# Kernel tuning notes

Measured on AMD Instinct MI355X. Metric: run time of the kernel, lower is better.

Reference implementation:

```python
import jax, jax.numpy as jnp
import numpy as np

CH = 512
HEADS = 8
REDUCTION = 2
INNER = max(CH // REDUCTION, HEADS)  # 256
POS_RES = 16
LN_EPS = 1e-5


def setup_inputs() -> dict:
    key = jax.random.key(0)
    ks = jax.random.split(key, 7)
    B, H, W = 1, 64, 64
    x = jax.random.normal(ks[0], (B, CH, H, W), dtype=jnp.float32)
    w_qkv = jax.random.normal(ks[1], (INNER * 3, CH), dtype=jnp.float32) * 0.02
    w_proj = jax.random.normal(ks[2], (CH, INNER), dtype=jnp.float32) * 0.02
    b_proj = jnp.zeros((CH,), dtype=jnp.float32)
    pos_bias = jax.random.normal(ks[3], (1, HEADS, POS_RES, POS_RES), dtype=jnp.float32) * 0.02
    gamma = jnp.ones((CH,), dtype=jnp.float32)
    beta = jnp.zeros((CH,), dtype=jnp.float32)
    return {"x": x, "w_qkv": w_qkv, "w_proj": w_proj, "b_proj": b_proj,
            "pos_bias": pos_bias, "gamma": gamma, "beta": beta}


def reference(x, w_qkv, w_proj, b_proj, pos_bias, gamma, beta):
    B, C, H, W = x.shape
    d_head = INNER // HEADS
    scale = jnp.float32(d_head ** -0.5)

    # 1x1 conv == channel matmul
    qkv = jnp.einsum('oc,bchw->bohw', w_qkv, x)  # [B, 3*inner, H, W]
    q, k, v = jnp.split(qkv, 3, axis=1)

    def heads_view(t):
        return t.reshape(B, HEADS, d_head, H * W)  # [B, h, d, HW]

    q, k, v = heads_view(q), heads_view(k), heads_view(v)

    attn = jnp.einsum('bhdi,bhdj->bhij', q * scale, k)  # [B, h, HW, HW]

    # bilinear interp of pos bias 16x16 -> HxW (half-pixel, matches align_corners=False)
    pos = jax.image.resize(pos_bias, (1, HEADS, H, W), method='bilinear')
    pos = pos.reshape(1, HEADS, H * W)
    attn = attn + pos[..., :, None] + pos[..., None, :]

    attn = jax.nn.softmax(attn, axis=-1)
    y = jnp.einsum('bhij,bhdj->bhdi', attn, v)  # [B, h, d, HW]
    y = y.reshape(B, INNER, H, W)

    y = jnp.einsum('co,bohw->bchw', w_proj, y) + b_proj[None, :, None, None]

    # LayerNorm over channel dim of (x + y)
    z = (x + y).transpose(0, 2, 3, 1)  # [B, H, W, C]
    mu = jnp.mean(z, axis=-1, keepdims=True)
    var = jnp.var(z, axis=-1, keepdims=True)
    z = (z - mu) / jnp.sqrt(var + LN_EPS) * gamma + beta
    return z.transpose(0, 3, 1, 2)
```

## Files before the change

### kernel.cpp

```cpp
#include <hip/hip_runtime.h>
#include <hip/hip_bf16.h>
#include <math.h>

#define HW 4096
#define LN_EPS 1e-5f

typedef _Float16 half4v __attribute__((ext_vector_type(4)));
typedef _Float16 half8v __attribute__((ext_vector_type(8)));
typedef float float4v __attribute__((ext_vector_type(4)));
typedef __fp16 fp16v2 __attribute__((ext_vector_type(2)));
typedef __fp16 fp16v4 __attribute__((ext_vector_type(4)));

#if __has_builtin(__builtin_amdgcn_exp2f)
#define EXP2F(x) __builtin_amdgcn_exp2f(x)
#else
#define EXP2F(x) exp2f(x)
#endif

__device__ __forceinline__ half4v lo4(half8v v) { return __builtin_shufflevector(v, v, 0, 1, 2, 3); }
__device__ __forceinline__ half4v hi4(half8v v) { return __builtin_shufflevector(v, v, 4, 5, 6, 7); }

__device__ __forceinline__ void gload_lds16(const _Float16* g, _Float16* l) {
#if __has_builtin(__builtin_amdgcn_global_load_lds)
    __builtin_amdgcn_global_load_lds(
        (const __attribute__((address_space(1))) void*)(const void*)g,
        (__attribute__((address_space(3))) void*)(void*)l, 16, 0, 0);
#else
    int lane = threadIdx.x & 63;
    *(half8v*)(l + lane * 8) = *(const half8v*)g;
#endif
}

__global__ __launch_bounds__(256) void k_pre(const float* __restrict__ x,
                                             const float* __restrict__ wq,
                                             const float* __restrict__ wp,
                                             const float* __restrict__ pb,
                                             _Float16* __restrict__ xt,
                                             _Float16* __restrict__ wqh,
                                             _Float16* __restrict__ wph,
                                             float* __restrict__ pos) {
    int bx = blockIdx.x, t = threadIdx.x;
    if (bx < 512) {
        __shared__ _Float16 tile[64][65];
        int c0 = (bx >> 6) * 64, p0 = (bx & 63) * 64;
        int w = t >> 6, lane = t & 63;
        #pragma unroll
        for (int r = 0; r < 16; r++)
            tile[w * 16 + r][lane] = (_Float16)x[(c0 + w * 16 + r) * HW + p0 + lane];
        __syncthreads();
        int cg = (t & 15) * 4, pr = t >> 4;
        #pragma unroll
        for (int r = 0; r < 4; r++) {
            int p = pr + r * 16;
            half4v v;
            #pragma unroll
            for (int k = 0; k < 4; k++) v[k] = tile[cg + k][p];
            *(half4v*)&xt[(p0 + p) * 512 + c0 + cg] = v;
        }
        return;
    }
    int i = (bx - 512) * 256 + t;
    const float qs = 0.17677669529663687f * 1.4426950408889634f;
    if (i < 49152) {
        float s = (i < 16384) ? qs : 1.0f;
        float4v a = *(const float4v*)(wq + i * 8);
        float4v b = *(const float4v*)(wq + i * 8 + 4);
        half8v h;
        #pragma unroll
        for (int k = 0; k < 4; k++) { h[k] = (_Float16)(a[k] * s); h[4 + k] = (_Float16)(b[k] * s); }
        *(half8v*)(wqh + i * 8) = h;
    } else if (i < 65536) {
        int j = i - 49152;
        float4v a = *(const float4v*)(wp + j * 8);
        float4v b = *(const float4v*)(wp + j * 8 + 4);
        half8v h;
        #pragma unroll
        for (int k = 0; k < 4; k++) { h[k] = (_Float16)a[k]; h[4 + k] = (_Float16)b[k]; }
        *(half8v*)(wph + j * 8) = h;
    } else {
        int j = i - 65536;
        int h = j >> 12, p = j & 4095, y = p >> 6, xx = p & 63;
        float sy = y * 0.25f - 0.375f, sx = xx * 0.25f - 0.375f;
        float fy = floorf(sy), fx = floorf(sx);
        float wy = sy - fy, wx = sx - fx;
        int y0 = (int)fy, x0 = (int)fx;
        int y1 = y0 + 1 < 15 ? y0 + 1 : 15;
        int x1 = x0 + 1 < 15 ? x0 + 1 : 15;
        y0 = y0 > 0 ? y0 : 0;
        x0 = x0 > 0 ? x0 : 0;
        const float* src = pb + h * 256;
        float v = (1.f - wy) * ((1.f - wx) * src[y0 * 16 + x0] + wx * src[y0 * 16 + x1]) +
                  wy * ((1.f - wx) * src[y1 * 16 + x0] + wx * src[y1 * 16 + x1]);
        pos[j] = v * 1.4426950408889634f;
    }
}

__global__ __launch_bounds__(256) void k_qkv(const _Float16* __restrict__ wqh,
                                             const _Float16* __restrict__ xt,
                                             _Float16* __restrict__ qa,
                                             _Float16* __restrict__ ka,
                                             _Float16* __restrict__ va) {
    int n0 = (blockIdx.x >> 5) * 64;
    int p0 = (blockIdx.x & 31) * 128;
    int t = threadIdx.x, w = t >> 6, lane = t & 63, quad = lane >> 4, l16 = lane & 15;

    const _Float16* aptr0 = xt + (p0 + w * 16 + l16) * 512 + quad * 8;
    const _Float16* aptr1 = aptr0 + 64 * 512;
    const _Float16* bptr = wqh + (n0 + l16) * 512 + quad * 8;

    float4v acc[2][4] = {};
    #pragma unroll 4
    for (int kc = 0; kc < 16; kc++) {
        half8v a0 = *(const half8v*)(aptr0 + kc * 32);
        half8v a1 = *(const half8v*)(aptr1 + kc * 32);
        #pragma unroll
        for (int nt = 0; nt < 4; nt++) {
            half8v b = *(const half8v*)(bptr + nt * 16 * 512 + kc * 32);
            acc[0][nt] = __builtin_amdgcn_mfma_f32_16x16x32_f16(a0, b, acc[0][nt], 0, 0, 0);
            acc[1][nt] = __builtin_amdgcn_mfma_f32_16x16x32_f16(a1, b, acc[1][nt], 0, 0, 0);
        }
    }
    #pragma unroll
    for (int ps = 0; ps < 2; ps++) {
        #pragma unroll
        for (int nt = 0; nt < 4; nt++) {
            int o = n0 + nt * 16 + l16;
            #pragma unroll
            for (int r = 0; r < 4; r++) {
                int p = p0 + ps * 64 + w * 16 + quad * 4 + r;
                _Float16 v = (_Float16)acc[ps][nt][r];
                if (o < 256) {
                    qa[(o >> 5) * 131072 + p * 32 + (o & 31)] = v;
                } else if (o < 512) {
                    int oc = o - 256, hh = oc >> 5, d = oc & 31;
                    ka[hh * 131072 + (p >> 4) * 512 + ((d >> 3) * 16 + (p & 15)) * 8 + (d & 7)] = v;
                } else {
                    int oc = o - 512, hh = oc >> 5, d = oc & 31;
                    va[hh * 131072 + (p >> 4) * 512 + (((p >> 2) & 3) * 16 + (d & 15)) * 8 +
                       (d >> 4) * 4 + (p & 3)] = v;
                }
            }
        }
    }
}

__global__ __launch_bounds__(256, 4) void k_attn(const _Float16* __restrict__ qa,
                                                 const _Float16* __restrict__ ka,
                                                 const _Float16* __restrict__ va,
                                                 const float* __restrict__ pos,
                                                 float* __restrict__ op,
                                                 float* __restrict__ lp) {
    __shared__ __attribute__((aligned(16))) _Float16 kbuf[2][2048];
    __shared__ __attribute__((aligned(16))) _Float16 vbuf[2][2048];
    __shared__ __attribute__((aligned(16))) float posl[1024];
    int h = blockIdx.x & 7;
    int jq = (blockIdx.x >> 3) & 3;
    int qb = blockIdx.x >> 5;
    int t = threadIdx.x, w = t >> 6, lane = t & 63, quad = lane >> 4, l16 = lane & 15;
    int q0 = qb * 128 + w * 32;

    float* opp = op + jq * 1048576;
    float* lpp = lp + jq * 32768;

    *(float4v*)(posl + t * 4) = *(const float4v*)(pos + h * HW + jq * 1024 + t * 4);

    half8v qf0 = *(const half8v*)(qa + h * 131072 + (q0 + l16) * 32 + quad * 8);
    half8v qf1 = *(const half8v*)(qa + h * 131072 + (q0 + 16 + l16) * 32 + quad * 8);

    const _Float16* kg = ka + h * 131072 + jq * 32768;
    const _Float16* vg = va + h * 131072 + jq * 32768;

    gload_lds16(kg + (w * 64 + lane) * 8, &kbuf[0][w * 512]);
    gload_lds16(vg + (w * 64 + lane) * 8, &vbuf[0][w * 512]);

    float4v o00 = {}, o01 = {}, o10 = {}, o11 = {};
    float lsum0 = 0.f, lsum1 = 0.f;
    const fp16v2 one2 = {(__fp16)1.0f, (__fp16)1.0f};

    for (int tile = 0; tile < 16; tile++) {
        int buf = tile & 1;
        __syncthreads();
        if (tile + 1 < 16) {
            gload_lds16(kg + (tile + 1) * 2048 + (w * 64 + lane) * 8, &kbuf[buf ^ 1][w * 512]);
            gload_lds16(vg + (tile + 1) * 2048 + (w * 64 + lane) * 8, &vbuf[buf ^ 1][w * 512]);
        }
        #pragma unroll
        for (int w16 = 0; w16 < 4; w16++) {
            half8v kf = *(const half8v*)(kbuf[buf] + w16 * 512 + lane * 8);
            half8v vf = *(const half8v*)(vbuf[buf] + w16 * 512 + lane * 8);
            float4v pbv = *(const float4v*)(posl + tile * 64 + w16 * 16 + quad * 4);

            float4v s0 = __builtin_amdgcn_mfma_f32_16x16x32_f16(kf, qf0, pbv, 0, 0, 0);
            float4v s1 = __builtin_amdgcn_mfma_f32_16x16x32_f16(kf, qf1, pbv, 0, 0, 0);

            float e0 = EXP2F(s0[0]);
            float e1 = EXP2F(s0[1]);
            float e2 = EXP2F(s0[2]);
            float e3 = EXP2F(s0[3]);
            float f0 = EXP2F(s1[0]);
            float f1 = EXP2F(s1[1]);
            float f2 = EXP2F(s1[2]);
            float f3 = EXP2F(s1[3]);

            fp16v2 a01 = __builtin_amdgcn_cvt_pkrtz(e0, e1);
            fp16v2 a23 = __builtin_amdgcn_cvt_pkrtz(e2, e3);
            fp16v2 b01 = __builtin_amdgcn_cvt_pkrtz(f0, f1);
            fp16v2 b23 = __builtin_amdgcn_cvt_pkrtz(f2, f3);
            half4v pa0 = __builtin_bit_cast(half4v, __builtin_shufflevector(a01, a23, 0, 1, 2, 3));
            half4v pa1 = __builtin_bit_cast(half4v, __builtin_shufflevector(b01, b23, 0, 1, 2, 3));

#if __has_builtin(__builtin_amdgcn_fdot2)
            lsum0 = __builtin_amdgcn_fdot2(a01, one2, lsum0, false);
            lsum0 = __builtin_amdgcn_fdot2(a23, one2, lsum0, false);
            lsum1 = __builtin_amdgcn_fdot2(b01, one2, lsum1, false);
            lsum1 = __builtin_amdgcn_fdot2(b23, one2, lsum1, false);
#else
            lsum0 += (e0 + e1) + (e2 + e3);
            lsum1 += (f0 + f1) + (f2 + f3);
#endif
            o00 = __builtin_amdgcn_mfma_f32_16x16x16f16(pa0, lo4(vf), o00, 0, 0, 0);
            o01 = __builtin_amdgcn_mfma_f32_16x16x16f16(pa0, hi4(vf), o01, 0, 0, 0);
            o10 = __builtin_amdgcn_mfma_f32_16x16x16f16(pa1, lo4(vf), o10, 0, 0, 0);
            o11 = __builtin_amdgcn_mfma_f32_16x16x16f16(pa1, hi4(vf), o11, 0, 0, 0);
        }
    }
    lsum0 += __shfl_xor(lsum0, 16, 64);
    lsum0 += __shfl_xor(lsum0, 32, 64);
    lsum1 += __shfl_xor(lsum1, 16, 64);
    lsum1 += __shfl_xor(lsum1, 32, 64);
    #pragma unroll
    for (int r = 0; r < 4; r++) {
        int qr = quad * 4 + r;
        int qi0 = q0 + qr, qi1 = q0 + 16 + qr;
        opp[qi0 * 256 + h * 32 + l16] = o00[r];
        opp[qi0 * 256 + h * 32 + 16 + l16] = o01[r];
        opp[qi1 * 256 + h * 32 + l16] = o10[r];
        opp[qi1 * 256 + h * 32 + 16 + l16] = o11[r];
    }
    if (quad == 0) {
        lpp[(q0 + l16) * 8 + h] = lsum0;
        lpp[(q0 + 16 + l16) * 8 + h] = lsum1;
    }
}

__global__ __launch_bounds__(1024) void k_proj_ln(const _Float16* __restrict__ wph,
                                                  const float* __restrict__ op,
                                                  const float* __restrict__ lp,
                                                  const float* __restrict__ x,
                                                  const float* __restrict__ b_proj,
                                                  const float* __restrict__ gamma,
                                                  const float* __restrict__ beta,
                                                  float* __restrict__ out) {
    __shared__ __attribute__((aligned(16))) _Float16 ys[16 * 264];
    __shared__ float red[2][16][17];
    int p0 = blockIdx.x * 16;
    int t = threadIdx.x, w = t >> 6, lane = t & 63, quad = lane >> 4, l16 = lane & 15;
    {
        int p = t >> 6, cg = (t & 63) * 4;
        int pi = p0 + p;
        float4v a0 = *(const float4v*)(op + pi * 256 + cg);
        float4v a1 = *(const float4v*)(op + 1048576 + pi * 256 + cg);
        float4v a2 = *(const float4v*)(op + 2097152 + pi * 256 + cg);
        float4v a3 = *(const float4v*)(op + 3145728 + pi * 256 + cg);
        int hh = cg >> 5;
        float l = lp[pi * 8 + hh] + lp[32768 + pi * 8 + hh] +
                  lp[65536 + pi * 8 + hh] + lp[98304 + pi * 8 + hh];
        float inv = 1.f / l;
        half4v y;
        #pragma unroll
        for (int k = 0; k < 4; k++) y[k] = (_Float16)(((a0[k] + a1[k]) + (a2[k] + a3[k])) * inv);
        *(half4v*)(ys + p * 264 + cg) = y;
    }
    __syncthreads();
    float4v acc[2] = {};
    #pragma unroll
    for (int kc = 0; kc < 8; kc++) {
        half8v b = *(const half8v*)(ys + l16 * 264 + kc * 32 + quad * 8);
        #pragma unroll
        for (int mt = 0; mt < 2; mt++) {
            half8v a = *(const half8v*)(wph + (w * 32 + mt * 16 + l16) * 256 + kc * 32 + quad * 8);
            acc[mt] = __builtin_amdgcn_mfma_f32_16x16x32_f16(a, b, acc[mt], 0, 0, 0);
        }
    }
    int p = p0 + l16;
    float sum = 0.f, sumsq = 0.f;
    #pragma unroll
    for (int mt = 0; mt < 2; mt++)
        #pragma unroll
        for (int r = 0; r < 4; r++) {
            int c = w * 32 + mt * 16 + quad * 4 + r;
            float v = acc[mt][r] + b_proj[c] + x[c * HW + p];
            acc[mt][r] = v;
            sum += v;
            sumsq += v * v;
        }
    sum += __shfl_xor(sum, 16, 64);
    sum += __shfl_xor(sum, 32, 64);
    sumsq += __shfl_xor(sumsq, 16, 64);
    sumsq += __shfl_xor(sumsq, 32, 64);
    if (quad == 0) { red[0][w][l16] = sum; red[1][w][l16] = sumsq; }
    __syncthreads();
    float s0 = 0.f, s1 = 0.f;
    #pragma unroll
    for (int ww = 0; ww < 16; ww++) { s0 += red[0][ww][l16]; s1 += red[1][ww][l16]; }
    float mean = s0 * (1.f / 512.f);
    float var = s1 * (1.f / 512.f) - mean * mean;
    float rstd = rsqrtf(var + LN_EPS);
    #pragma unroll
    for (int mt = 0; mt < 2; mt++)
        #pragma unroll
        for (int r = 0; r < 4; r++) {
            int c = w * 32 + mt * 16 + quad * 4 + r;
            out[c * HW + p] = (acc[mt][r] - mean) * rstd * gamma[c] + beta[c];
        }
}

extern "C" void kernel_launch(void* const* d_in, const int* in_sizes, int n_in,
                              void* d_out, int out_size, void* d_ws, size_t ws_size,
                              hipStream_t stream) {
    const float* x      = (const float*)d_in[0];
    const float* w_qkv  = (const float*)d_in[1];
    const float* w_proj = (const float*)d_in[2];
    const float* b_proj = (const float*)d_in[3];
    const float* pos_b  = (const float*)d_in[4];
    const float* gamma  = (const float*)d_in[5];
    const float* beta   = (const float*)d_in[6];
    char* ws = (char*)d_ws;
    _Float16* xt  = (_Float16*)(ws);
    _Float16* qa  = (_Float16*)(ws + 4194304);
    _Float16* ka  = (_Float16*)(ws + 6291456);
    _Float16* va  = (_Float16*)(ws + 8388608);
    float*    op  = (float*)   (ws + 10485760);
    float*    lp  = (float*)   (ws + 27262976);
    float*    pos = (float*)   (ws + 27787264);
    _Float16* wqh = (_Float16*)(ws + 27918336);
    _Float16* wph = (_Float16*)(ws + 28704768);

    k_pre<<<896, 256, 0, stream>>>(x, w_qkv, w_proj, pos_b, xt, wqh, wph, pos);
    k_qkv<<<384, 256, 0, stream>>>(wqh, xt, qa, ka, va);
    k_attn<<<1024, 256, 0, stream>>>(qa, ka, va, pos, op, lp);
    k_proj_ln<<<256, 1024, 0, stream>>>(wph, op, lp, x, b_proj, gamma, beta, (float*)d_out);
}
```

Baseline: 140.3 us.

## Use 16x16x32 MFMA for PV by re-laying K/V in 32-key pairs, store partials in fp16

```diff
diff --git a/kernel.cpp b/kernel.cpp
--- a/kernel.cpp
+++ b/kernel.cpp
@@ -16,9 +16,6 @@
 #else
 #define EXP2F(x) exp2f(x)
 #endif
-
-__device__ __forceinline__ half4v lo4(half8v v) { return __builtin_shufflevector(v, v, 0, 1, 2, 3); }
-__device__ __forceinline__ half4v hi4(half8v v) { return __builtin_shufflevector(v, v, 4, 5, 6, 7); }
 
 __device__ __forceinline__ void gload_lds16(const _Float16* g, _Float16* l) {
 #if __has_builtin(__builtin_amdgcn_global_load_lds)
@@ -133,11 +130,16 @@
                     qa[(o >> 5) * 131072 + p * 32 + (o & 31)] = v;
                 } else if (o < 512) {
                     int oc = o - 256, hh = oc >> 5, d = oc & 31;
-                    ka[hh * 131072 + (p >> 4) * 512 + ((d >> 3) * 16 + (p & 15)) * 8 + (d & 7)] = v;
+                    int p5 = p & 31, pair = p >> 5;
+                    int window = (p5 >> 2) & 1;
+                    int localrow = (p5 >> 3) * 4 + (p5 & 3);
+                    ka[hh * 131072 + (pair * 2 + window) * 512 +
+                       ((d >> 3) * 16 + localrow) * 8 + (d & 7)] = v;
                 } else {
                     int oc = o - 512, hh = oc >> 5, d = oc & 31;
-                    va[hh * 131072 + (p >> 4) * 512 + (((p >> 2) & 3) * 16 + (d & 15)) * 8 +
-                       (d >> 4) * 4 + (p & 3)] = v;
+                    int p5 = p & 31, pair = p >> 5;
+                    va[hh * 131072 + pair * 1024 + (d >> 4) * 512 +
+                       ((p5 >> 3) * 16 + (d & 15)) * 8 + (p5 & 7)] = v;
                 }
             }
         }
@@ -148,10 +150,10 @@
                                                  const _Float16* __restrict__ ka,
                                                  const _Float16* __restrict__ va,
                                                  const float* __restrict__ pos,
-                                                 float* __restrict__ op,
+                                                 _Float16* __restrict__ op,
                                                  float* __restrict__ lp) {
-    __shared__ __attribute__((aligned(16))) _Float16 kbuf[2][2048];
-    __shared__ __attribute__((aligned(16))) _Float16 vbuf[2][2048];
+    __shared__ __attribute__((aligned(16))) _Float16 kbuf[2][4096];
+    __shared__ __attribute__((aligned(16))) _Float16 vbuf[2][4096];
     __shared__ __attribute__((aligned(16))) float posl[1024];
     int h = blockIdx.x & 7;
     int jq = (blockIdx.x >> 3) & 3;
@@ -159,7 +161,7 @@
     int t = threadIdx.x, w = t >> 6, lane = t & 63, quad = lane >> 4, l16 = lane & 15;
     int q0 = qb * 128 + w * 32;
 
-    float* opp = op + jq * 1048576;
+    _Float16* opp = op + jq * 1048576;
     float* lpp = lp + jq * 32768;
 
     *(float4v*)(posl + t * 4) = *(const float4v*)(pos + h * HW + jq * 1024 + t * 4);
@@ -171,57 +173,79 @@
     const _Float16* vg = va + h * 131072 + jq * 32768;
 
     gload_lds16(kg + (w * 64 + lane) * 8, &kbuf[0][w * 512]);
+    gload_lds16(kg + 2048 + (w * 64 + lane) * 8, &kbuf[0][2048 + w * 512]);
     gload_lds16(vg + (w * 64 + lane) * 8, &vbuf[0][w * 512]);
+    gload_lds16(vg + 2048 + (w * 64 + lane) * 8, &vbuf[0][2048 + w * 512]);
 
     float4v o00 = {}, o01 = {}, o10 = {}, o11 = {};
     float lsum0 = 0.f, lsum1 = 0.f;
     const fp16v2 one2 = {(__fp16)1.0f, (__fp16)1.0f};
 
-    for (int tile = 0; tile < 16; tile++) {
+    for (int tile = 0; tile < 8; tile++) {
         int buf = tile & 1;
         __syncthreads();
-        if (tile + 1 < 16) {
-            gload_lds16(kg + (tile + 1) * 2048 + (w * 64 + lane) * 8, &kbuf[buf ^ 1][w * 512]);
-            gload_lds16(vg + (tile + 1) * 2048 + (w * 64 + lane) * 8, &vbuf[buf ^ 1][w * 512]);
-        }
-        #pragma unroll
-        for (int w16 = 0; w16 < 4; w16++) {
-            half8v kf = *(const half8v*)(kbuf[buf] + w16 * 512 + lane * 8);
-            half8v vf = *(const half8v*)(vbuf[buf] + w16 * 512 + lane * 8);
-            float4v pbv = *(const float4v*)(posl + tile * 64 + w16 * 16 + quad * 4);
-
-            float4v s0 = __builtin_amdgcn_mfma_f32_16x16x32_f16(kf, qf0, pbv, 0, 0, 0);
-            float4v s1 = __builtin_amdgcn_mfma_f32_16x16x32_f16(kf, qf1, pbv, 0, 0, 0);
-
-            float e0 = EXP2F(s0[0]);
-            float e1 = EXP2F(s0[1]);
-            float e2 = EXP2F(s0[2]);
-            float e3 = EXP2F(s0[3]);
-            float f0 = EXP2F(s1[0]);
-            float f1 = EXP2F(s1[1]);
-            float f2 = EXP2F(s1[2]);
-            float f3 = EXP2F(s1[3]);
+        if (tile + 1 < 8) {
+            const _Float16* kn = kg + (tile + 1) * 4096;
+            const _Float16* vn = vg + (tile + 1) * 4096;
+            gload_lds16(kn + (w * 64 + lane) * 8, &kbuf[buf ^ 1][w * 512]);
+            gload_lds16(kn + 2048 + (w * 64 + lane) * 8, &kbuf[buf ^ 1][2048 + w * 512]);
+            gload_lds16(vn + (w * 64 + lane) * 8, &vbuf[buf ^ 1][w * 512]);
+            gload_lds16(vn + 2048 + (w * 64 + lane) * 8, &vbuf[buf ^ 1][2048 + w * 512]);
+        }
+        #pragma unroll
+        for (int pp = 0; pp < 4; pp++) {
+            const _Float16* kb = &kbuf[buf][pp * 1024];
+            const _Float16* vb = &vbuf[buf][pp * 1024];
+            half8v kf0 = *(const half8v*)(kb + lane * 8);
+            half8v kf1 = *(const half8v*)(kb + 512 + lane * 8);
+            half8v vlo = *(const half8v*)(vb + lane * 8);
+            half8v vhi = *(const half8v*)(vb + 512 + lane * 8);
+            float4v pb0 = *(const float4v*)(posl + tile * 128 + pp * 32 + quad * 8);
+            float4v pb1 = *(const float4v*)(posl + tile * 128 + pp * 32 + quad * 8 + 4);
+
+            float4v s00 = __builtin_amdgcn_mfma_f32_16x16x32_f16(kf0, qf0, pb0, 0, 0, 0);
+            float4v s01 = __builtin_amdgcn_mfma_f32_16x16x32_f16(kf0, qf1, pb0, 0, 0, 0);
+            float4v s10 = __builtin_amdgcn_mfma_f32_16x16x32_f16(kf1, qf0, pb1, 0, 0, 0);
+            float4v s11 = __builtin_amdgcn_mfma_f32_16x16x32_f16(kf1, qf1, pb1, 0, 0, 0);
+
+            float e0 = EXP2F(s00[0]), e1 = EXP2F(s00[1]), e2 = EXP2F(s00[2]), e3 = EXP2F(s00[3]);
+            float e4 = EXP2F(s10[0]), e5 = EXP2F(s10[1]), e6 = EXP2F(s10[2]), e7 = EXP2F(s10[3]);
+            float f0 = EXP2F(s01[0]), f1 = EXP2F(s01[1]), f2 = EXP2F(s01[2]), f3 = EXP2F(s01[3]);
+            float f4 = EXP2F(s11[0]), f5 = EXP2F(s11[1]), f6 = EXP2F(s11[2]), f7 = EXP2F(s11[3]);
 
             fp16v2 a01 = __builtin_amdgcn_cvt_pkrtz(e0, e1);
             fp16v2 a23 = __builtin_amdgcn_cvt_pkrtz(e2, e3);
+            fp16v2 a45 = __builtin_amdgcn_cvt_pkrtz(e4, e5);
+            fp16v2 a67 = __builtin_amdgcn_cvt_pkrtz(e6, e7);
             fp16v2 b01 = __builtin_amdgcn_cvt_pkrtz(f0, f1);
             fp16v2 b23 = __builtin_amdgcn_cvt_pkrtz(f2, f3);
-            half4v pa0 = __builtin_bit_cast(half4v, __builtin_shufflevector(a01, a23, 0, 1, 2, 3));
-            half4v pa1 = __builtin_bit_cast(half4v, __builtin_shufflevector(b01, b23, 0, 1, 2, 3));
+            fp16v2 b45 = __builtin_amdgcn_cvt_pkrtz(f4, f5);
+            fp16v2 b67 = __builtin_amdgcn_cvt_pkrtz(f6, f7);
+
+            half4v pA0 = __builtin_bit_cast(half4v, __builtin_shufflevector(a01, a23, 0, 1, 2, 3));
+            half4v pA1 = __builtin_bit_cast(half4v, __builtin_shufflevector(a45, a67, 0, 1, 2, 3));
+            half8v pa0 = __builtin_shufflevector(pA0, pA1, 0, 1, 2, 3, 4, 5, 6, 7);
+            half4v pB0 = __builtin_bit_cast(half4v, __builtin_shufflevector(b01, b23, 0, 1, 2, 3));
+            half4v pB1 = __builtin_bit_cast(half4v, __builtin_shufflevector(b45, b67, 0, 1, 2, 3));
+            half8v pa1 = __builtin_shufflevector(pB0, pB1, 0, 1, 2, 3, 4, 5, 6, 7);
 
 #if __has_builtin(__builtin_amdgcn_fdot2)
             lsum0 = __builtin_amdgcn_fdot2(a01, one2, lsum0, false);
             lsum0 = __builtin_amdgcn_fdot2(a23, one2, lsum0, false);
+            lsum0 = __builtin_amdgcn_fdot2(a45, one2, lsum0, false);
+            lsum0 = __builtin_amdgcn_fdot2(a67, one2, lsum0, false);
             lsum1 = __builtin_amdgcn_fdot2(b01, one2, lsum1, false);
             lsum1 = __builtin_amdgcn_fdot2(b23, one2, lsum1, false);
+            lsum1 = __builtin_amdgcn_fdot2(b45, one2, lsum1, false);
+            lsum1 = __builtin_amdgcn_fdot2(b67, one2, lsum1, false);
 #else
-            lsum0 += (e0 + e1) + (e2 + e3);
-            lsum1 += (f0 + f1) + (f2 + f3);
+            lsum0 += ((e0 + e1) + (e2 + e3)) + ((e4 + e5) + (e6 + e7));
+            lsum1 += ((f0 + f1) + (f2 + f3)) + ((f4 + f5) + (f6 + f7));
 #endif
-            o00 = __builtin_amdgcn_mfma_f32_16x16x16f16(pa0, lo4(vf), o00, 0, 0, 0);
-            o01 = __builtin_amdgcn_mfma_f32_16x16x16f16(pa0, hi4(vf), o01, 0, 0, 0);
-            o10 = __builtin_amdgcn_mfma_f32_16x16x16f16(pa1, lo4(vf), o10, 0, 0, 0);
-            o11 = __builtin_amdgcn_mfma_f32_16x16x16f16(pa1, hi4(vf), o11, 0, 0, 0);
+            o00 = __builtin_amdgcn_mfma_f32_16x16x32_f16(pa0, vlo, o00, 0, 0, 0);
+            o01 = __builtin_amdgcn_mfma_f32_16x16x32_f16(pa0, vhi, o01, 0, 0, 0);
+            o10 = __builtin_amdgcn_mfma_f32_16x16x32_f16(pa1, vlo, o10, 0, 0, 0);
+            o11 = __builtin_amdgcn_mfma_f32_16x16x32_f16(pa1, vhi, o11, 0, 0, 0);
         }
     }
     lsum0 += __shfl_xor(lsum0, 16, 64);
@@ -232,10 +256,10 @@
     for (int r = 0; r < 4; r++) {
         int qr = quad * 4 + r;
         int qi0 = q0 + qr, qi1 = q0 + 16 + qr;
-        opp[qi0 * 256 + h * 32 + l16] = o00[r];
-        opp[qi0 * 256 + h * 32 + 16 + l16] = o01[r];
-        opp[qi1 * 256 + h * 32 + l16] = o10[r];
-        opp[qi1 * 256 + h * 32 + 16 + l16] = o11[r];
+        opp[qi0 * 256 + h * 32 + l16] = (_Float16)o00[r];
+        opp[qi0 * 256 + h * 32 + 16 + l16] = (_Float16)o01[r];
+        opp[qi1 * 256 + h * 32 + l16] = (_Float16)o10[r];
+        opp[qi1 * 256 + h * 32 + 16 + l16] = (_Float16)o11[r];
     }
     if (quad == 0) {
         lpp[(q0 + l16) * 8 + h] = lsum0;
@@ -244,7 +268,7 @@
 }
 
 __global__ __launch_bounds__(1024) void k_proj_ln(const _Float16* __restrict__ wph,
-                                                  const float* __restrict__ op,
+                                                  const _Float16* __restrict__ op,
                                                   const float* __restrict__ lp,
                                                   const float* __restrict__ x,
                                                   const float* __restrict__ b_proj,
@@ -258,17 +282,19 @@
     {
         int p = t >> 6, cg = (t & 63) * 4;
         int pi = p0 + p;
-        float4v a0 = *(const float4v*)(op + pi * 256 + cg);
-        float4v a1 = *(const float4v*)(op + 1048576 + pi * 256 + cg);
-        float4v a2 = *(const float4v*)(op + 2097152 + pi * 256 + cg);
-        float4v a3 = *(const float4v*)(op + 3145728 + pi * 256 + cg);
+        half4v a0 = *(const half4v*)(op + pi * 256 + cg);
+        half4v a1 = *(const half4v*)(op + 1048576 + pi * 256 + cg);
+        half4v a2 = *(const half4v*)(op + 2097152 + pi * 256 + cg);
+        half4v a3 = *(const half4v*)(op + 3145728 + pi * 256 + cg);
         int hh = cg >> 5;
         float l = lp[pi * 8 + hh] + lp[32768 + pi * 8 + hh] +
                   lp[65536 + pi * 8 + hh] + lp[98304 + pi * 8 + hh];
         float inv = 1.f / l;
         half4v y;
         #pragma unroll
-        for (int k = 0; k < 4; k++) y[k] = (_Float16)(((a0[k] + a1[k]) + (a2[k] + a3[k])) * inv);
+        for (int k = 0; k < 4; k++)
+            y[k] = (_Float16)((((float)a0[k] + (float)a1[k]) +
+                               ((float)a2[k] + (float)a3[k])) * inv);
         *(half4v*)(ys + p * 264 + cg) = y;
     }
     __syncthreads();
@@ -330,11 +356,11 @@
     _Float16* qa  = (_Float16*)(ws + 4194304);
     _Float16* ka  = (_Float16*)(ws + 6291456);
     _Float16* va  = (_Float16*)(ws + 8388608);
-    float*    op  = (float*)   (ws + 10485760);
-    float*    lp  = (float*)   (ws + 27262976);
-    float*    pos = (float*)   (ws + 27787264);
-    _Float16* wqh = (_Float16*)(ws + 27918336);
-    _Float16* wph = (_Float16*)(ws + 28704768);
+    _Float16* op  = (_Float16*)(ws + 10485760);
+    float*    lp  = (float*)   (ws + 18874368);
+    float*    pos = (float*)   (ws + 19398656);
+    _Float16* wqh = (_Float16*)(ws + 19529728);
+    _Float16* wph = (_Float16*)(ws + 20316160);
 
     k_pre<<<896, 256, 0, stream>>>(x, w_qkv, w_proj, pos_b, xt, wqh, wph, pos);
     k_qkv<<<384, 256, 0, stream>>>(wqh, xt, qa, ka, va);
```

After: 135.1 us. 1.04x faster.
